# Performance work log

Measured on AMD Instinct MI355X. Metric: run time of the kernel, lower is better.

## Reference

```python
import jax, jax.numpy as jnp
import numpy as np

B, S, H, W, C = 2, 21, 256, 256, 256
Q, NEG = 256, 256
TEMP = 0.5
STRONG_T = 1.0
EPS = 1e-8


def setup_inputs():
    key = jax.random.key(0)
    k1, k2, k3 = jax.random.split(key, 3)
    rep = jax.random.normal(k1, (B, C, H, W), jnp.float32)
    label = jax.random.randint(k2, (B, 1, H, W), 0, S)
    mask = jnp.ones((B, 1, H, W), jnp.float32)
    prob = jax.random.uniform(k3, (B, S, H, W), jnp.float32)
    return {"rep": rep, "label": label, "mask": mask, "prob": prob}


def _cos(a, b, axis=-1):
    # torch.cosine_similarity: dot / (max(|a|,eps) * max(|b|,eps))
    an = jnp.maximum(jnp.linalg.norm(a, axis=axis), EPS)
    bn = jnp.maximum(jnp.linalg.norm(b, axis=axis), EPS)
    return jnp.sum(a * b, axis=axis) / (an * bn)


def _reco_loss(rep, label, mask, prob):
    Sg = prob.shape[1]
    Cf = rep.shape[1]
    lab = label.reshape(-1).astype(jnp.int32)          # [N]
    ignore = lab > Sg - 1
    lab = jnp.where(ignore, 0, lab)
    m = jnp.where(ignore, 0.0, mask.reshape(-1))
    valid = m > 0                                      # [N]
    feats = jnp.transpose(rep, (0, 2, 3, 1)).reshape(-1, Cf)   # [N,C]
    pflat = jnp.transpose(prob, (0, 2, 3, 1)).reshape(-1, Sg)  # [N,S]
    p_lab = jnp.take_along_axis(pflat, lab[:, None], axis=1)[:, 0]
    hard = valid & (p_lab < STRONG_T)

    seg_id = jnp.where(valid, lab, Sg)  # invalid pixels -> overflow bucket Sg
    counts = jax.ops.segment_sum(valid.astype(jnp.int32), seg_id, num_segments=Sg + 1)[:Sg]
    hard_counts = jax.ops.segment_sum(hard.astype(jnp.int32), seg_id, num_segments=Sg + 1)[:Sg]
    proto = jax.ops.segment_sum(feats * valid[:, None].astype(feats.dtype), seg_id,
                                num_segments=Sg + 1)[:Sg]
    proto = proto / jnp.maximum(counts, 1)[:, None].astype(feats.dtype)  # [S,C]

    # stable sort pixels by (segment, hard-first): emulates the per-segment
    # boolean-mask gathers / concatenation order of the torch code
    order = jnp.argsort(seg_id * 2 + (~hard).astype(jnp.int32))
    feats_sorted = feats[order]                                 # [N,C]
    off = jnp.concatenate([jnp.zeros((1,), counts.dtype), jnp.cumsum(counts)[:-1]])

    seg_ids = jnp.arange(Sg)
    keys = jax.random.split(jax.random.key(1), Sg)

    def body(acc, xs):
        i, ki = xs
        ka, kc, kn = jax.random.split(ki, 3)
        # anchors: num_queries random hard pixels of segment i
        hidx = off[i] + jax.random.randint(ka, (Q,), 0, jnp.maximum(hard_counts[i], 1))
        anchor = feats_sorted[hidx]                             # [Q,C]
        # negative class distribution over other segments (rolled order)
        roll = (i + 1 + jnp.arange(Sg - 1)) % Sg
        proto_logits = _cos(proto[i][None, :], proto[roll]) / TEMP  # [S-1]
        samp = jax.random.categorical(kc, proto_logits, shape=(Q, NEG))
        neg_seg = roll[samp]                                    # [Q,NEG]
        # uniform pixel within each sampled segment's block
        u = jax.random.uniform(kn, (Q, NEG))
        nidx = off[neg_seg] + jnp.floor(u * jnp.maximum(counts[neg_seg], 1)).astype(counts.dtype)
        neg_feat = feats_sorted[nidx]                           # [Q,NEG,C]
        all_feat = jnp.concatenate(
            [jnp.broadcast_to(proto[i], (Q, 1, Cf)), neg_feat], axis=1)
        all_feat = jax.lax.stop_gradient(all_feat)              # torch.no_grad block
        seg_logits = _cos(anchor[:, None, :], all_feat) / TEMP  # [Q,1+NEG]
        # cross-entropy with target 0, mean over queries
        ce = jnp.mean(jax.nn.logsumexp(seg_logits, axis=1) - seg_logits[:, 0])
        acc = acc + jnp.where(hard_counts[i] > 0, ce, 0.0)
        return acc, None

    total, _ = jax.lax.scan(body, jnp.float32(0.0), (seg_ids, keys))
    valid_seg = jnp.sum(counts > 0)
    loss = total / jnp.maximum(valid_seg, 1).astype(jnp.float32)
    return jnp.where(valid_seg > 1, loss, jnp.float32(0.0))


def reference(rep, label, mask, prob):
    loss_weight = 1.0
    return loss_weight * _reco_loss(rep, label, mask, prob)
```

## Files before the change

kernel.cpp:

```cpp
#include <hip/hip_runtime.h>
#include <stdint.h>

#define NPIX  131072
#define HW    65536
#define CCH   256
#define NSEG  21
#define NROLL 20

typedef float f32x2 __attribute__((ext_vector_type(2)));
typedef __fp16 half2t __attribute__((ext_vector_type(2)));

__device__ __forceinline__ uint64_t rng64(uint32_t i, uint32_t q, uint32_t j) {
  uint64_t x = ((uint64_t)((i << 8) | q) << 32) | (uint64_t)(j * 0x9E3779B1u);
  x ^= 0xD1B54A32D192ED03ULL;
  x += 0x9E3779B97F4A7C15ULL;
  x = (x ^ (x >> 30)) * 0xBF58476D1CE4E5B9ULL;
  x = (x ^ (x >> 27)) * 0x94D049BB133111EBULL;
  return x ^ (x >> 31);
}

__device__ __forceinline__ float fdot2h(half2t a, half2t b, float c) {
  return __builtin_amdgcn_fdot2(a, b, c, false);
}

__device__ __forceinline__ void dec16(uint4 w, half2t* nx) {
  uint32_t dw[4] = { w.x, w.y, w.z, w.w };
#pragma unroll
  for (int d = 0; d < 4; ++d) {
    f32x2 lo = __builtin_amdgcn_cvt_pk_f32_fp8((int)dw[d], false);
    f32x2 hi = __builtin_amdgcn_cvt_pk_f32_fp8((int)dw[d], true);
    nx[d * 2 + 0] = __builtin_amdgcn_cvt_pkrtz(lo.x, lo.y);
    nx[d * 2 + 1] = __builtin_amdgcn_cvt_pkrtz(hi.x, hi.y);
  }
}

__global__ __launch_bounds__(256) void reco_flags(
    const int* __restrict__ label, const float* __restrict__ mask,
    const float* __restrict__ prob, int* __restrict__ labh,
    int* __restrict__ bc, float4* __restrict__ zr) {
  int row = blockIdx.x;
  int b = row >> 8;
  int h = row & 255;
  int t = threadIdx.x;
  int n = row * 256 + t;

  if (row < 6) {
    int idx = row * 256 + t;
    if (idx < 1360) zr[idx] = make_float4(0.f, 0.f, 0.f, 0.f);
  }

  int lab = label[n];
  bool ignore = lab > NSEG - 1;
  if (ignore) lab = 0;
  float mval = ignore ? 0.f : mask[n];
  bool valid = mval > 0.f;
  float p_lab = prob[(((size_t)b * NSEG + lab) * 256 + h) * 256 + t];
  bool hard = valid && (p_lab < 1.0f);
  labh[n] = lab | (hard ? 32 : 0) | (valid ? 64 : 0);

  __shared__ int cpart[NSEG], hpart[NSEG];
  if (t < NSEG) { cpart[t] = 0; hpart[t] = 0; }
  __syncthreads();
  if (valid) { atomicAdd(&cpart[lab], 1); if (hard) atomicAdd(&hpart[lab], 1); }
  __syncthreads();
  if (t < NSEG) {
    bc[t * 512 + row] = cpart[t];
    bc[(24 + t) * 512 + row] = hpart[t];
  }
}

__global__ __launch_bounds__(256) void reco_k2t(
    const int* __restrict__ bc, int* __restrict__ counts, int* __restrict__ hardc,
    int* __restrict__ offs, int* __restrict__ cur_h, int* __restrict__ cur_e) {
  int t = threadIdx.x;
  int wave = t >> 6, lane = t & 63;
  __shared__ int sums[42];
  for (int c = wave; c < 42; c += 4) {
    int col = (c < 21) ? c : c + 3;
    const int* p = bc + col * 512 + lane * 8;
    int s = 0;
#pragma unroll
    for (int j = 0; j < 8; ++j) s += p[j];
#pragma unroll
    for (int o = 32; o >= 1; o >>= 1) s += __shfl_xor(s, o);
    if (lane == 0) sums[c] = s;
  }
  __syncthreads();
  if (t == 0) {
    int o = 0;
    for (int s = 0; s < NSEG; ++s) {
      counts[s] = sums[s];
      hardc[s] = sums[21 + s];
      offs[s] = o;
      cur_h[s] = o;
      cur_e[s] = o + sums[21 + s];
      o += sums[s];
    }
    offs[NSEG] = o;
  }
}

__global__ __launch_bounds__(256) void reco_k3(const int* __restrict__ labh,
                        int* __restrict__ cur_h, int* __restrict__ cur_e, int* __restrict__ list) {
  int t = threadIdx.x;
  int n = blockIdx.x * 256 + t;
  __shared__ int lcnt[2 * NSEG];
  __shared__ int lbase[2 * NSEG];
  if (t < 2 * NSEG) lcnt[t] = 0;
  __syncthreads();
  int v = labh[n];
  int lab = v & 31;
  bool hard = (v & 32) != 0;
  bool valid = (v & 64) != 0;
  int bucket = lab + (hard ? 0 : NSEG);
  int rank = 0;
  if (valid) rank = atomicAdd(&lcnt[bucket], 1);
  __syncthreads();
  if (t < 2 * NSEG) {
    int c = lcnt[t];
    lbase[t] = c ? atomicAdd((t < NSEG) ? &cur_h[t] : &cur_e[t - NSEG], c) : 0;
  }
  __syncthreads();
  if (valid) list[lbase[bucket] + rank] = n;
}

__global__ __launch_bounds__(256) void reco_k5f(const float* __restrict__ rep,
                        uint8_t* __restrict__ f8, float* __restrict__ norms) {
  int bid = blockIdx.x;
  int wtile = bid & 3;
  int row = bid >> 2;
  int b = row >> 8, h = row & 255;
  int w0 = wtile * 64;
  int t = threadIdx.x;

  __shared__ float tile[64][257];
  __shared__ float partial[4][64];
  __shared__ float inv[64];

  const float* repb = rep + (size_t)b * CCH * HW + (size_t)h * 256 + w0;
  int w4 = t & 15;
  int cbase = t >> 4;
#pragma unroll
  for (int it = 0; it < 16; ++it) {
    int c = it * 16 + cbase;
    float4 v = *(const float4*)&repb[(size_t)c * HW + w4 * 4];
    tile[w4 * 4 + 0][c] = v.x;
    tile[w4 * 4 + 1][c] = v.y;
    tile[w4 * 4 + 2][c] = v.z;
    tile[w4 * 4 + 3][c] = v.w;
  }
  __syncthreads();

  {
    int w = t & 63, qtr = t >> 6;
    float acc = 0.f;
#pragma unroll 8
    for (int cc = 0; cc < 64; ++cc) {
      float v = tile[w][qtr * 64 + cc];
      acc += v * v;
    }
    partial[qtr][w] = acc;
  }
  __syncthreads();
  if (t < 64) {
    float s = partial[0][t] + partial[1][t] + partial[2][t] + partial[3][t];
    float nm = fmaxf(sqrtf(s), 1e-8f);
    inv[t] = 1.0f / nm;
    norms[row * 256 + w0 + t] = nm;
  }
  __syncthreads();

  int pix = t & 7, chunk = t >> 3;
#pragma unroll
  for (int it = 0; it < 8; ++it) {
    int p = it * 8 + pix;
    float iv = inv[p];
    float v[8];
#pragma unroll
    for (int k = 0; k < 8; ++k) v[k] = tile[p][chunk * 8 + k] * iv;
    uint32_t lo = 0, hi = 0;
    lo = (uint32_t)__builtin_amdgcn_cvt_pk_fp8_f32(v[0], v[1], (int)lo, false);
    lo = (uint32_t)__builtin_amdgcn_cvt_pk_fp8_f32(v[2], v[3], (int)lo, true);
    hi = (uint32_t)__builtin_amdgcn_cvt_pk_fp8_f32(v[4], v[5], (int)hi, false);
    hi = (uint32_t)__builtin_amdgcn_cvt_pk_fp8_f32(v[6], v[7], (int)hi, true);
    size_t n = (size_t)(row * 256 + w0 + p);
    uint2 o; o.x = lo; o.y = hi;
    *(uint2*)&f8[n * CCH + chunk * 8] = o;
  }
}

__global__ __launch_bounds__(256) void reco_proto8(
    const uint8_t* __restrict__ f8, const float* __restrict__ norms,
    const int* __restrict__ list, const int* __restrict__ labh,
    const int* __restrict__ offs, float* __restrict__ proto) {
  int t = threadIdx.x;
  int base = blockIdx.x * 256;
  int total = offs[NSEG];

  __shared__ uint8_t rows[64][256];
  __shared__ float nrm[64];
  __shared__ int segs[256];
  __shared__ int pixs[256];
  __shared__ float red[64][17];

  {
    int pos = base + t;
    int p = (pos < total) ? (list[pos] & (NPIX - 1)) : -1;
    pixs[t] = p;
    segs[t] = (p >= 0) ? (labh[p] & 31) : -1;
  }
  __syncthreads();

  int d = t & 63;
  int qt = t >> 6;
  float a0 = 0.f, a1 = 0.f, a2 = 0.f, a3 = 0.f;
  int cseg = -2;

  for (int sub = 0; sub < 4; ++sub) {
    {
      int r = t >> 2, c = (t & 3) * 64;
      int p = pixs[sub * 64 + r];
      uint4* dst = (uint4*)&rows[r][c];
      if (p >= 0) {
        const uint4* src = (const uint4*)&f8[(size_t)p * CCH + c];
        dst[0] = src[0]; dst[1] = src[1]; dst[2] = src[2]; dst[3] = src[3];
      } else {
        uint4 z = make_uint4(0, 0, 0, 0);
        dst[0] = z; dst[1] = z; dst[2] = z; dst[3] = z;
      }
      if (t < 64) {
        int pp = pixs[sub * 64 + t];
        nrm[t] = (pp >= 0) ? norms[pp] : 0.f;
      }
    }
    __syncthreads();
    for (int pp = 0; pp < 16; ++pp) {
      int pl = qt * 16 + pp;
      int sg = segs[sub * 64 + pl];
      if (sg >= 0) {
        if (sg != cseg) {
          if (cseg >= 0) {
            atomicAdd(&proto[cseg * CCH + d * 4 + 0], a0);
            atomicAdd(&proto[cseg * CCH + d * 4 + 1], a1);
            atomicAdd(&proto[cseg * CCH + d * 4 + 2], a2);
            atomicAdd(&proto[cseg * CCH + d * 4 + 3], a3);
          }
          a0 = a1 = a2 = a3 = 0.f;
          cseg = sg;
        }
        uint32_t w = *(const uint32_t*)&rows[pl][d * 4];
        f32x2 lo = __builtin_amdgcn_cvt_pk_f32_fp8((int)w, false);
        f32x2 hi = __builtin_amdgcn_cvt_pk_f32_fp8((int)w, true);
        float nv = nrm[pl];
        a0 += lo.x * nv; a1 += lo.y * nv; a2 += hi.x * nv; a3 += hi.y * nv;
      }
    }
    __syncthreads();
  }

  int s0 = segs[0];
  int uni = __syncthreads_and((cseg < 0) || (cseg == s0));
  if (uni) {
    if (cseg >= 0) {
      red[d][qt * 4 + 0] = a0;
      red[d][qt * 4 + 1] = a1;
      red[d][qt * 4 + 2] = a2;
      red[d][qt * 4 + 3] = a3;
    }
    __syncthreads();
    if (t < 64 && s0 >= 0) {
#pragma unroll
      for (int c = 0; c < 4; ++c) {
        float v = red[t][0 + c] + red[t][4 + c] + red[t][8 + c] + red[t][12 + c];
        atomicAdd(&proto[s0 * CCH + t * 4 + c], v);
      }
    }
  } else if (cseg >= 0) {
    atomicAdd(&proto[cseg * CCH + d * 4 + 0], a0);
    atomicAdd(&proto[cseg * CCH + d * 4 + 1], a1);
    atomicAdd(&proto[cseg * CCH + d * 4 + 2], a2);
    atomicAdd(&proto[cseg * CCH + d * 4 + 3], a3);
  }
}

__global__ __launch_bounds__(256) void reco_k4(float* __restrict__ proto, float* __restrict__ protoN,
                        const int* __restrict__ counts, float* __restrict__ cdf) {
  __shared__ float pn[NSEG];
  __shared__ float spN[NSEG * CCH];
  __shared__ float lg[NSEG][NROLL];
  int t = threadIdx.x;
  for (int idx = t; idx < NSEG * CCH; idx += 256) {
    int s = idx >> 8;
    int c = counts[s]; if (c < 1) c = 1;
    proto[idx] = proto[idx] / (float)c;
  }
  __syncthreads();
  if (t < NSEG) {
    float s2 = 0.f;
    for (int c = 0; c < CCH; ++c) { float v = proto[t * CCH + c]; s2 += v * v; }
    pn[t] = fmaxf(sqrtf(s2), 1e-8f);
  }
  __syncthreads();
  for (int idx = t; idx < NSEG * CCH; idx += 256) {
    int s = idx >> 8;
    float v = proto[idx] / pn[s];
    spN[idx] = v;
    protoN[idx] = v;
  }
  __syncthreads();
  for (int idx = t; idx < NSEG * NROLL; idx += 256) {
    int i = idx / NROLL, k = idx % NROLL;
    int j = (i + 1 + k) % NSEG;
    float d = 0.f;
    for (int c = 0; c < CCH; ++c) d += spN[i * CCH + c] * spN[j * CCH + c];
    lg[i][k] = d * 2.0f;
  }
  __syncthreads();
  if (t < NSEG) {
    float mx = -1e30f;
    for (int k = 0; k < NROLL; ++k) mx = fmaxf(mx, lg[t][k]);
    float e[NROLL]; float s = 0.f;
    for (int k = 0; k < NROLL; ++k) { e[k] = __expf(lg[t][k] - mx); s += e[k]; }
    float a = 0.f;
    for (int k = 0; k < NROLL; ++k) { a += e[k] / s; cdf[t * NROLL + k] = a; }
    cdf[t * NROLL + NROLL - 1] = 2.0f;
  }
}

__global__ __launch_bounds__(256) void reco_k6r(
    const uint8_t* __restrict__ f8, const int* __restrict__ list,
    const int* __restrict__ counts, const int* __restrict__ hardc,
    const int* __restrict__ offs, const float* __restrict__ protoN,
    const float* __restrict__ cdf, float* __restrict__ seg_sum,
    int* __restrict__ ticket, float* __restrict__ out) {
  int bid = blockIdx.x;
  int i  = bid >> 5;
  int qc = bid & 31;
  int t = threadIdx.x;

  __shared__ half2t anch[8 * 128];
  __shared__ float pNs[256];
  __shared__ float lgts[8][264];
  __shared__ float s_cdf[NROLL];
  __shared__ int s_off[NSEG], s_cnt[NSEG], s_pidx[256], s_apix[8];
  __shared__ float s_ce[8];
  __shared__ int s_last;

  if (t < NSEG) { s_off[t] = offs[t]; s_cnt[t] = counts[t]; }
  if (t < NROLL) s_cdf[t] = cdf[i * NROLL + t];
  pNs[t] = protoN[i * CCH + t];
  if (t < 8) {
    int q = qc * 8 + t;
    uint64_t r = rng64(i, q, 511u);
    int hc = hardc[i]; if (hc < 1) hc = 1;
    uint32_t jj = (uint32_t)(r & 0xffffffffu) % (uint32_t)hc;
    int idx = offs[i] + (int)jj;
    if (idx > NPIX - 1) idx = NPIX - 1;
    s_apix[t] = list[idx] & (NPIX - 1);
  }
  __syncthreads();

  {
    uint64_t r = rng64(i, 0u, (uint32_t)(t + 1));
    float u1 = (float)(r >> 40) * (1.0f / 16777216.0f);
    float u2 = (float)((r >> 16) & 0xFFFFFFu) * (1.0f / 16777216.0f);
    int k = 0;
#pragma unroll
    for (int kk = 0; kk < NROLL - 1; ++kk) k += (u1 >= s_cdf[kk]);
    int seg = i + 1 + k; if (seg >= NSEG) seg -= NSEG;
    int cnt = s_cnt[seg]; int cm = cnt < 1 ? 1 : cnt;
    int pidx = (int)(u2 * (float)cm);
    if (pidx > cm - 1) pidx = cm - 1;
    int li = s_off[seg] + pidx;
    if (li > NPIX - 1) li = NPIX - 1;
    s_pidx[t] = list[li] & (NPIX - 1);
  }
  if (t < 128) {
    int g = t >> 4, x = t & 15;
    uint4 w = *(const uint4*)&f8[(size_t)s_apix[g] * CCH + x * 16];
    half2t dx[8]; dec16(w, dx);
#pragma unroll
    for (int k = 0; k < 8; ++k) anch[g * 128 + x * 8 + k] = dx[k];
  }
  __syncthreads();

  const uint4* rowp = (const uint4*)&f8[(size_t)s_pidx[t] * CCH];
  float acc[8];
#pragma unroll
  for (int q = 0; q < 8; ++q) acc[q] = 0.f;
  for (int k0 = 0; k0 < 16; k0 += 4) {
    uint4 w4[4];
#pragma unroll
    for (int u = 0; u < 4; ++u) w4[u] = rowp[k0 + u];
#pragma unroll
    for (int u = 0; u < 4; ++u) {
      half2t nx[8]; dec16(w4[u], nx);
      const half2t* ar = anch + (k0 + u) * 8;
#pragma unroll
      for (int q = 0; q < 8; ++q) {
        const half2t* a = ar + q * 128;
        float s = acc[q];
#pragma unroll
        for (int k = 0; k < 8; ++k) s = fdot2h(a[k], nx[k], s);
        acc[q] = s;
      }
    }
  }
  float ps = 0.f;
  if (t < 128) {
    int g = t >> 4, x = t & 15;
#pragma unroll
    for (int k = 0; k < 8; ++k) {
      half2t a = anch[g * 128 + x * 8 + k];
      ps += (float)a.x * pNs[x * 16 + 2 * k] + (float)a.y * pNs[x * 16 + 2 * k + 1];
    }
#pragma unroll
    for (int o = 1; o <= 8; o <<= 1) ps += __shfl_xor(ps, o);
  }

#pragma unroll
  for (int q = 0; q < 8; ++q) lgts[q][1 + t] = acc[q] * 2.0f;
  if (t < 128 && (t & 15) == 0) lgts[t >> 4][0] = ps * 2.0f;
  __syncthreads();

  int wave = t >> 6, lane = t & 63;
  for (int q = wave; q < 8; q += 4) {
    const float* L = lgts[q];
    float v0 = L[lane], v1 = L[lane + 64], v2 = L[lane + 128], v3 = L[lane + 192];
    float v4 = (lane == 0) ? L[256] : -1e30f;
    float m = fmaxf(fmaxf(fmaxf(v0, v1), fmaxf(v2, v3)), v4);
#pragma unroll
    for (int o = 32; o >= 1; o >>= 1) m = fmaxf(m, __shfl_xor(m, o));
    float e = __expf(v0 - m) + __expf(v1 - m) + __expf(v2 - m) + __expf(v3 - m)
            + ((lane == 0) ? __expf(v4 - m) : 0.f);
#pragma unroll
    for (int o = 32; o >= 1; o >>= 1) e += __shfl_xor(e, o);
    if (lane == 0) s_ce[q] = m + logf(e) - L[0];
  }
  __syncthreads();
  if (t == 0) {
    float s = 0.f;
#pragma unroll
    for (int q = 0; q < 8; ++q) s += s_ce[q];
    atomicAdd(&seg_sum[i], s);
    __threadfence();
    int done = atomicAdd(ticket, 1);
    s_last = (done == NSEG * 32 - 1);
  }
  __syncthreads();
  if (s_last && t == 0) {
    __threadfence();
    float tot = 0.f; int vs = 0;
    for (int s = 0; s < NSEG; ++s) {
      vs += (counts[s] > 0);
      float v = atomicAdd(&seg_sum[s], 0.f);
      if (hardc[s] > 0) tot += v;
    }
    float loss = (tot * (1.0f / 256.0f)) / (float)(vs > 0 ? vs : 1);
    out[0] = (vs > 1) ? loss : 0.f;
  }
}

extern "C" void kernel_launch(void* const* d_in, const int* in_sizes, int n_in,
                              void* d_out, int out_size, void* d_ws, size_t ws_size,
                              hipStream_t stream) {
  const float* rep   = (const float*)d_in[0];
  const int*   label = (const int*)d_in[1];
  const float* mask  = (const float*)d_in[2];
  const float* prob  = (const float*)d_in[3];

  char* ws = (char*)d_ws;
  uint8_t* f8 = (uint8_t*)ws;
  size_t o = 67108864;
  float* norms  = (float*)(ws + o); o += 524288;
  int*   list   = (int*)(ws + o);   o += 524288;
  int*   labh   = (int*)(ws + o);   o += 524288;
  float* proto  = (float*)(ws + o); o += 21504;
  float* segsum = (float*)(ws + o); o += 128;
  int*   ticket = (int*)(ws + o);   o += 128;
  int*   counts = (int*)(ws + o);   o += 128;
  int*   hardc  = (int*)(ws + o);   o += 128;
  int*   offs   = (int*)(ws + o);   o += 128;
  int*   cur_h  = (int*)(ws + o);   o += 128;
  int*   cur_e  = (int*)(ws + o);   o += 128;
  float* protoN = (float*)(ws + o); o += 21504;
  float* cdf    = (float*)(ws + o); o += 2048;
  int*   bc     = (int*)(ws + o);   o += 98304;

  reco_flags<<<512, 256, 0, stream>>>(label, mask, prob, labh, bc, (float4*)proto);
  reco_k2t<<<1, 256, 0, stream>>>(bc, counts, hardc, offs, cur_h, cur_e);
  reco_k3<<<512, 256, 0, stream>>>(labh, cur_h, cur_e, list);
  reco_k5f<<<2048, 256, 0, stream>>>(rep, f8, norms);
  reco_proto8<<<512, 256, 0, stream>>>(f8, norms, list, labh, offs, proto);
  reco_k4<<<1, 256, 0, stream>>>(proto, protoN, counts, cdf);
  reco_k6r<<<NSEG * 32, 256, 0, stream>>>(f8, list, counts, hardc, offs,
                                          protoN, cdf, segsum, ticket, (float*)d_out);
}
```

Baseline: 123.6 us.

## Merge flags and fp8 feature kernels, fold prototype normalization into loss kernel

Combines the label/flag pass and the rep-to-fp8 normalization pass into one launch, choosing the branch by block index. The single-block prototype normalization and CDF kernel is removed, and every loss block now recomputes the normalized prototypes and its own segment's sampling CDF in shared memory. This cuts two kernel launches and the serial single-block step. In exchange, each of the 672 loss blocks repeats the prototype normalization and uses more shared memory, which may lower occupancy. The flag blocks also now reserve the large shared allocation they do not need.

New measurement: 106.6 us. -13.7%, faster.

```diff
diff --git a/kernel.cpp b/kernel.cpp
--- a/kernel.cpp
+++ b/kernel.cpp
@@ -34,38 +34,98 @@
   }
 }
 
-__global__ __launch_bounds__(256) void reco_flags(
-    const int* __restrict__ label, const float* __restrict__ mask,
-    const float* __restrict__ prob, int* __restrict__ labh,
-    int* __restrict__ bc, float4* __restrict__ zr) {
-  int row = blockIdx.x;
-  int b = row >> 8;
-  int h = row & 255;
+__global__ __launch_bounds__(256) void reco_a(
+    const float* __restrict__ rep, const int* __restrict__ label,
+    const float* __restrict__ mask, const float* __restrict__ prob,
+    uint8_t* __restrict__ f8, float* __restrict__ norms,
+    int* __restrict__ labh, int* __restrict__ bc, float4* __restrict__ zr) {
   int t = threadIdx.x;
-  int n = row * 256 + t;
-
-  if (row < 6) {
-    int idx = row * 256 + t;
-    if (idx < 1360) zr[idx] = make_float4(0.f, 0.f, 0.f, 0.f);
-  }
-
-  int lab = label[n];
-  bool ignore = lab > NSEG - 1;
-  if (ignore) lab = 0;
-  float mval = ignore ? 0.f : mask[n];
-  bool valid = mval > 0.f;
-  float p_lab = prob[(((size_t)b * NSEG + lab) * 256 + h) * 256 + t];
-  bool hard = valid && (p_lab < 1.0f);
-  labh[n] = lab | (hard ? 32 : 0) | (valid ? 64 : 0);
-
-  __shared__ int cpart[NSEG], hpart[NSEG];
-  if (t < NSEG) { cpart[t] = 0; hpart[t] = 0; }
-  __syncthreads();
-  if (valid) { atomicAdd(&cpart[lab], 1); if (hard) atomicAdd(&hpart[lab], 1); }
-  __syncthreads();
-  if (t < NSEG) {
-    bc[t * 512 + row] = cpart[t];
-    bc[(24 + t) * 512 + row] = hpart[t];
+  __shared__ __align__(16) char SM[68352];
+
+  if (blockIdx.x < 2048) {
+    float* tile = (float*)SM;
+    float* partial = (float*)(SM + 65792);
+    float* inv = (float*)(SM + 66816);
+    int bid = blockIdx.x;
+    int wtile = bid & 3;
+    int row = bid >> 2;
+    int b = row >> 8, h = row & 255;
+    int w0 = wtile * 64;
+
+    const float* repb = rep + (size_t)b * CCH * HW + (size_t)h * 256 + w0;
+    int w4 = t & 15, cbase = t >> 4;
+#pragma unroll
+    for (int it = 0; it < 16; ++it) {
+      int c = it * 16 + cbase;
+      float4 v = *(const float4*)&repb[(size_t)c * HW + w4 * 4];
+      tile[(w4 * 4 + 0) * 257 + c] = v.x;
+      tile[(w4 * 4 + 1) * 257 + c] = v.y;
+      tile[(w4 * 4 + 2) * 257 + c] = v.z;
+      tile[(w4 * 4 + 3) * 257 + c] = v.w;
+    }
+    __syncthreads();
+    {
+      int w = t & 63, qtr = t >> 6;
+      float acc = 0.f;
+#pragma unroll 8
+      for (int cc = 0; cc < 64; ++cc) {
+        float v = tile[w * 257 + qtr * 64 + cc];
+        acc += v * v;
+      }
+      partial[qtr * 64 + w] = acc;
+    }
+    __syncthreads();
+    if (t < 64) {
+      float s = partial[0 * 64 + t] + partial[1 * 64 + t] + partial[2 * 64 + t] + partial[3 * 64 + t];
+      float nm = fmaxf(sqrtf(s), 1e-8f);
+      inv[t] = 1.0f / nm;
+      norms[row * 256 + w0 + t] = nm;
+    }
+    __syncthreads();
+    int pix = t & 7, chunk = t >> 3;
+#pragma unroll
+    for (int it = 0; it < 8; ++it) {
+      int p = it * 8 + pix;
+      float iv = inv[p];
+      float v[8];
+#pragma unroll
+      for (int k = 0; k < 8; ++k) v[k] = tile[p * 257 + chunk * 8 + k] * iv;
+      uint32_t lo = 0, hi = 0;
+      lo = (uint32_t)__builtin_amdgcn_cvt_pk_fp8_f32(v[0], v[1], (int)lo, false);
+      lo = (uint32_t)__builtin_amdgcn_cvt_pk_fp8_f32(v[2], v[3], (int)lo, true);
+      hi = (uint32_t)__builtin_amdgcn_cvt_pk_fp8_f32(v[4], v[5], (int)hi, false);
+      hi = (uint32_t)__builtin_amdgcn_cvt_pk_fp8_f32(v[6], v[7], (int)hi, true);
+      size_t n = (size_t)(row * 256 + w0 + p);
+      uint2 o; o.x = lo; o.y = hi;
+      *(uint2*)&f8[n * CCH + chunk * 8] = o;
+    }
+  } else {
+    int row = blockIdx.x - 2048;
+    int b = row >> 8, h = row & 255;
+    int n = row * 256 + t;
+    if (row < 6) {
+      int idx = row * 256 + t;
+      if (idx < 1360) zr[idx] = make_float4(0.f, 0.f, 0.f, 0.f);
+    }
+    int lab = label[n];
+    bool ignore = lab > NSEG - 1;
+    if (ignore) lab = 0;
+    float mval = ignore ? 0.f : mask[n];
+    bool valid = mval > 0.f;
+    float p_lab = prob[(((size_t)b * NSEG + lab) * 256 + h) * 256 + t];
+    bool hard = valid && (p_lab < 1.0f);
+    labh[n] = lab | (hard ? 32 : 0) | (valid ? 64 : 0);
+
+    int* cpart = (int*)SM;
+    int* hpart = (int*)SM + 24;
+    if (t < NSEG) { cpart[t] = 0; hpart[t] = 0; }
+    __syncthreads();
+    if (valid) { atomicAdd(&cpart[lab], 1); if (hard) atomicAdd(&hpart[lab], 1); }
+    __syncthreads();
+    if (t < NSEG) {
+      bc[t * 512 + row] = cpart[t];
+      bc[(24 + t) * 512 + row] = hpart[t];
+    }
   }
 }
 
@@ -124,71 +184,6 @@
   if (valid) list[lbase[bucket] + rank] = n;
 }
 
-__global__ __launch_bounds__(256) void reco_k5f(const float* __restrict__ rep,
-                        uint8_t* __restrict__ f8, float* __restrict__ norms) {
-  int bid = blockIdx.x;
-  int wtile = bid & 3;
-  int row = bid >> 2;
-  int b = row >> 8, h = row & 255;
-  int w0 = wtile * 64;
-  int t = threadIdx.x;
-
-  __shared__ float tile[64][257];
-  __shared__ float partial[4][64];
-  __shared__ float inv[64];
-
-  const float* repb = rep + (size_t)b * CCH * HW + (size_t)h * 256 + w0;
-  int w4 = t & 15;
-  int cbase = t >> 4;
-#pragma unroll
-  for (int it = 0; it < 16; ++it) {
-    int c = it * 16 + cbase;
-    float4 v = *(const float4*)&repb[(size_t)c * HW + w4 * 4];
-    tile[w4 * 4 + 0][c] = v.x;
-    tile[w4 * 4 + 1][c] = v.y;
-    tile[w4 * 4 + 2][c] = v.z;
-    tile[w4 * 4 + 3][c] = v.w;
-  }
-  __syncthreads();
-
-  {
-    int w = t & 63, qtr = t >> 6;
-    float acc = 0.f;
-#pragma unroll 8
-    for (int cc = 0; cc < 64; ++cc) {
-      float v = tile[w][qtr * 64 + cc];
-      acc += v * v;
-    }
-    partial[qtr][w] = acc;
-  }
-  __syncthreads();
-  if (t < 64) {
-    float s = partial[0][t] + partial[1][t] + partial[2][t] + partial[3][t];
-    float nm = fmaxf(sqrtf(s), 1e-8f);
-    inv[t] = 1.0f / nm;
-    norms[row * 256 + w0 + t] = nm;
-  }
-  __syncthreads();
-
-  int pix = t & 7, chunk = t >> 3;
-#pragma unroll
-  for (int it = 0; it < 8; ++it) {
-    int p = it * 8 + pix;
-    float iv = inv[p];
-    float v[8];
-#pragma unroll
-    for (int k = 0; k < 8; ++k) v[k] = tile[p][chunk * 8 + k] * iv;
-    uint32_t lo = 0, hi = 0;
-    lo = (uint32_t)__builtin_amdgcn_cvt_pk_fp8_f32(v[0], v[1], (int)lo, false);
-    lo = (uint32_t)__builtin_amdgcn_cvt_pk_fp8_f32(v[2], v[3], (int)lo, true);
-    hi = (uint32_t)__builtin_amdgcn_cvt_pk_fp8_f32(v[4], v[5], (int)hi, false);
-    hi = (uint32_t)__builtin_amdgcn_cvt_pk_fp8_f32(v[6], v[7], (int)hi, true);
-    size_t n = (size_t)(row * 256 + w0 + p);
-    uint2 o; o.x = lo; o.y = hi;
-    *(uint2*)&f8[n * CCH + chunk * 8] = o;
-  }
-}
-
 __global__ __launch_bounds__(256) void reco_proto8(
     const uint8_t* __restrict__ f8, const float* __restrict__ norms,
     const int* __restrict__ list, const int* __restrict__ labh,
@@ -211,8 +206,7 @@
   }
   __syncthreads();
 
-  int d = t & 63;
-  int qt = t >> 6;
+  int d = t & 63, qt = t >> 6;
   float a0 = 0.f, a1 = 0.f, a2 = 0.f, a3 = 0.f;
   int cseg = -2;
 
@@ -283,63 +277,20 @@
   }
 }
 
-__global__ __launch_bounds__(256) void reco_k4(float* __restrict__ proto, float* __restrict__ protoN,
-                        const int* __restrict__ counts, float* __restrict__ cdf) {
-  __shared__ float pn[NSEG];
-  __shared__ float spN[NSEG * CCH];
-  __shared__ float lg[NSEG][NROLL];
-  int t = threadIdx.x;
-  for (int idx = t; idx < NSEG * CCH; idx += 256) {
-    int s = idx >> 8;
-    int c = counts[s]; if (c < 1) c = 1;
-    proto[idx] = proto[idx] / (float)c;
-  }
-  __syncthreads();
-  if (t < NSEG) {
-    float s2 = 0.f;
-    for (int c = 0; c < CCH; ++c) { float v = proto[t * CCH + c]; s2 += v * v; }
-    pn[t] = fmaxf(sqrtf(s2), 1e-8f);
-  }
-  __syncthreads();
-  for (int idx = t; idx < NSEG * CCH; idx += 256) {
-    int s = idx >> 8;
-    float v = proto[idx] / pn[s];
-    spN[idx] = v;
-    protoN[idx] = v;
-  }
-  __syncthreads();
-  for (int idx = t; idx < NSEG * NROLL; idx += 256) {
-    int i = idx / NROLL, k = idx % NROLL;
-    int j = (i + 1 + k) % NSEG;
-    float d = 0.f;
-    for (int c = 0; c < CCH; ++c) d += spN[i * CCH + c] * spN[j * CCH + c];
-    lg[i][k] = d * 2.0f;
-  }
-  __syncthreads();
-  if (t < NSEG) {
-    float mx = -1e30f;
-    for (int k = 0; k < NROLL; ++k) mx = fmaxf(mx, lg[t][k]);
-    float e[NROLL]; float s = 0.f;
-    for (int k = 0; k < NROLL; ++k) { e[k] = __expf(lg[t][k] - mx); s += e[k]; }
-    float a = 0.f;
-    for (int k = 0; k < NROLL; ++k) { a += e[k] / s; cdf[t * NROLL + k] = a; }
-    cdf[t * NROLL + NROLL - 1] = 2.0f;
-  }
-}
-
 __global__ __launch_bounds__(256) void reco_k6r(
     const uint8_t* __restrict__ f8, const int* __restrict__ list,
     const int* __restrict__ counts, const int* __restrict__ hardc,
-    const int* __restrict__ offs, const float* __restrict__ protoN,
-    const float* __restrict__ cdf, float* __restrict__ seg_sum,
-    int* __restrict__ ticket, float* __restrict__ out) {
+    const int* __restrict__ offs, const float* __restrict__ proto,
+    float* __restrict__ seg_sum, int* __restrict__ ticket, float* __restrict__ out) {
   int bid = blockIdx.x;
   int i  = bid >> 5;
   int qc = bid & 31;
   int t = threadIdx.x;
 
+  __shared__ float spN[NSEG * CCH];
+  __shared__ float pn[NSEG];
+  __shared__ float lgrow[NROLL];
   __shared__ half2t anch[8 * 128];
-  __shared__ float pNs[256];
   __shared__ float lgts[8][264];
   __shared__ float s_cdf[NROLL];
   __shared__ int s_off[NSEG], s_cnt[NSEG], s_pidx[256], s_apix[8];
@@ -347,8 +298,41 @@
   __shared__ int s_last;
 
   if (t < NSEG) { s_off[t] = offs[t]; s_cnt[t] = counts[t]; }
-  if (t < NROLL) s_cdf[t] = cdf[i * NROLL + t];
-  pNs[t] = protoN[i * CCH + t];
+  __syncthreads();
+
+  for (int idx = t; idx < NSEG * CCH; idx += 256) {
+    int s = idx >> 8;
+    int c = s_cnt[s]; if (c < 1) c = 1;
+    spN[idx] = proto[idx] / (float)c;
+  }
+  __syncthreads();
+  if (t < NSEG) {
+    float s2 = 0.f;
+    for (int c = 0; c < CCH; ++c) { float v = spN[t * CCH + c]; s2 += v * v; }
+    pn[t] = fmaxf(sqrtf(s2), 1e-8f);
+  }
+  __syncthreads();
+  for (int idx = t; idx < NSEG * CCH; idx += 256) {
+    int s = idx >> 8;
+    spN[idx] = spN[idx] / pn[s];
+  }
+  __syncthreads();
+  if (t < NROLL) {
+    int j = (i + 1 + t) % NSEG;
+    float d = 0.f;
+    for (int c = 0; c < CCH; ++c) d += spN[i * CCH + c] * spN[j * CCH + c];
+    lgrow[t] = d * 2.0f;
+  }
+  __syncthreads();
+  if (t == 0) {
+    float mx = -1e30f;
+    for (int k = 0; k < NROLL; ++k) mx = fmaxf(mx, lgrow[k]);
+    float e[NROLL]; float s = 0.f;
+    for (int k = 0; k < NROLL; ++k) { e[k] = __expf(lgrow[k] - mx); s += e[k]; }
+    float a = 0.f;
+    for (int k = 0; k < NROLL; ++k) { a += e[k] / s; s_cdf[k] = a; }
+    s_cdf[NROLL - 1] = 2.0f;
+  }
   if (t < 8) {
     int q = qc * 8 + t;
     uint64_t r = rng64(i, q, 511u);
@@ -409,6 +393,7 @@
   float ps = 0.f;
   if (t < 128) {
     int g = t >> 4, x = t & 15;
+    const float* pNs = spN + i * CCH;
 #pragma unroll
     for (int k = 0; k < 8; ++k) {
       half2t a = anch[g * 128 + x * 8 + k];
@@ -483,16 +468,12 @@
   int*   offs   = (int*)(ws + o);   o += 128;
   int*   cur_h  = (int*)(ws + o);   o += 128;
   int*   cur_e  = (int*)(ws + o);   o += 128;
-  float* protoN = (float*)(ws + o); o += 21504;
-  float* cdf    = (float*)(ws + o); o += 2048;
   int*   bc     = (int*)(ws + o);   o += 98304;
 
-  reco_flags<<<512, 256, 0, stream>>>(label, mask, prob, labh, bc, (float4*)proto);
+  reco_a<<<2560, 256, 0, stream>>>(rep, label, mask, prob, f8, norms, labh, bc, (float4*)proto);
   reco_k2t<<<1, 256, 0, stream>>>(bc, counts, hardc, offs, cur_h, cur_e);
   reco_k3<<<512, 256, 0, stream>>>(labh, cur_h, cur_e, list);
-  reco_k5f<<<2048, 256, 0, stream>>>(rep, f8, norms);
   reco_proto8<<<512, 256, 0, stream>>>(f8, norms, list, labh, offs, proto);
-  reco_k4<<<1, 256, 0, stream>>>(proto, protoN, counts, cdf);
-  reco_k6r<<<NSEG * 32, 256, 0, stream>>>(f8, list, counts, hardc, offs,
-                                          protoN, cdf, segsum, ticket, (float*)d_out);
-}
+  reco_k6r<<<NSEG * 32, 256, 0, stream>>>(f8, list, counts, hardc, offs, proto,
+                                          segsum, ticket, (float*)d_out);
+}
```
